# Performance work log

Measured on AMD Instinct MI355X. Metric: run time of the kernel, lower is better.

## Reference

```python
import jax, jax.numpy as jnp
import numpy as np

N = 320   # batch of events
D = 64    # features per event
P = 1000  # permutation_count (hard-coded in module)


def setup_inputs() -> dict:
    key = jax.random.key(0)
    k1, k2, k3 = jax.random.split(key, 3)
    data = jax.random.normal(k1, (N, D), dtype=jnp.float32)
    particle_types = jax.random.randint(k2, (N,), 0, 2, dtype=jnp.int32)
    # quantum permutations: 1000 independent random permutations of [0, N)
    perms = jax.vmap(lambda k: jax.random.permutation(k, N))(jax.random.split(k3, P)).astype(jnp.int32)
    return {
        "data": data,
        "fermion_antisymmetry": jnp.float32(-1.0),
        "boson_symmetry": jnp.float32(1.0),
        "particle_types": particle_types,
        "perms": perms,
    }


def reference(data, fermion_antisymmetry, boson_symmetry, particle_types, perms):
    n = data.shape[0]
    tf = particle_types  # [n]
    # statistics factor matrix F[i,j]: fermion-fermion -> -1 param, boson-boson -> +1 param, mixed -> 1.0
    ff = (tf[:, None] == 0) & (tf[None, :] == 0)
    bb = (tf[:, None] == 1) & (tf[None, :] == 1)
    F = jnp.where(ff, fermion_antisymmetry, jnp.where(bb, boson_symmetry, jnp.float32(1.0)))  # [n,n]

    ar = jnp.arange(n)
    gathered = data[perms]                      # [P,n,d] = data[perm[i]]
    fac = F[ar[None, :], perms]                 # [P,n]   = F[i, perm[i]]
    same = perms == ar[None, :]                 # i == perm[i]: keep original row unscaled
    perm_data = jnp.where(same[..., None], gathered, fac[..., None] * gathered)  # [P,n,d]

    all_data = jnp.concatenate([data[None], perm_data], axis=0)  # [P+1,n,d]; row 0 = original

    # pairwise Euclidean norms via Gram trick (avoids [P+1,n,n,d] diff tensor)
    sn = jnp.sum(all_data * all_data, axis=-1)                   # [P+1,n]
    gram = jnp.einsum('pnd,pmd->pnm', all_data, all_data)        # [P+1,n,n]
    sq = jnp.maximum(sn[:, :, None] + sn[:, None, :] - 2.0 * gram, 0.0)

    iu, ju = jnp.triu_indices(n, k=1)
    vals = F[iu, ju][None, :] * jnp.sqrt(sq[:, iu, ju])          # [P+1, n*(n-1)/2]
    # torch.var default is unbiased (ddof=1)
    stats = jnp.var(vals, axis=1, ddof=1)                        # [P+1]
    return stats  # stats[0] = original test statistic, stats[1:] = permutation null distribution
```

## Files before the change

kernel.cpp:

```cpp
#include <hip/hip_runtime.h>
#include <math.h>

#define NN 320
#define DD 64
#define ROWF (NN * 2)
#define NPERM 1001
#define KPB 4
#define NBLK ((NPERM + KPB - 1) / KPB)
#define NW 10
#define NITER 20
#define NPAIRF ((double)(NN * (NN - 1) / 2))


__global__ __launch_bounds__(NN) void dah_kernel(const float* __restrict__ data,
                                                 float2* __restrict__ DAH,
                                                 double* __restrict__ srow,
                                                 double* __restrict__ rsda) {
    __shared__ float rowa[DD];
    __shared__ double cr[5];
    const int a = blockIdx.x;
    const int t = threadIdx.x;
    if (t < DD) rowa[t] = data[a * DD + t];
    __syncthreads();
    const float* rb = data + t * DD;
    float g = 0.f, sa = 0.f, st = 0.f;
#pragma unroll
    for (int k = 0; k < DD; k += 4) {
        const float4 x = *(const float4*)(rb + k);
        const float r0 = rowa[k], r1 = rowa[k + 1], r2 = rowa[k + 2], r3 = rowa[k + 3];
        g  = fmaf(r0, x.x, g);   g  = fmaf(r1, x.y, g);
        g  = fmaf(r2, x.z, g);   g  = fmaf(r3, x.w, g);
        sa = fmaf(r0, r0, sa);   sa = fmaf(r1, r1, sa);
        sa = fmaf(r2, r2, sa);   sa = fmaf(r3, r3, sa);
        st = fmaf(x.x, x.x, st); st = fmaf(x.y, x.y, st);
        st = fmaf(x.z, x.z, st); st = fmaf(x.w, x.w, st);
    }
    const float sum = sa + st;
    const float dp = sqrtf(fmaxf(fmaf(-2.f, g, sum), 0.f));
    const float dm = sqrtf(fmaxf(fmaf( 2.f, g, sum), 0.f));
    const float da = 0.5f * (dp + dm);
    const float dh = 0.5f * (dp - dm);
    DAH[(size_t)a * NN + t] = make_float2(da, dh);

    double cd = (double)da;
    for (int off = 32; off; off >>= 1) cd += __shfl_down(cd, off, 64);
    const int wid = t >> 6, lane = t & 63;
    if (lane == 0) cr[wid] = cd;
    __syncthreads();
    if (t == 0) {
        double tot = 0.0;
#pragma unroll
        for (int i = 0; i < 5; ++i) tot += cr[i];
        rsda[a] = tot;
        srow[a] = (double)sa;
    }
}

__global__ __launch_bounds__(1024) void qf_kernel(const float* __restrict__ data,
                                                  const int* __restrict__ types,
                                                  const int* __restrict__ perms,
                                                  const float* __restrict__ fermp,
                                                  const float* __restrict__ bosp,
                                                  const float* __restrict__ DAHf,
                                                  const double* __restrict__ srow,
                                                  const double* __restrict__ rsda,
                                                  float* __restrict__ out) {
    __shared__ unsigned cb[KPB][2 * NW];
    __shared__ __align__(16) float rcoef[NN * 20];
    __shared__ float ysh[KPB][4][DD];
    __shared__ double red[16][12];
    __shared__ double redS[16], redC[16], scal[KPB];

    const int pg = blockIdx.x;
    const int t  = threadIdx.x;
    const int strip  = t & 63;
    const int rowoff = t >> 6;

    const float* gp = DAHf + (size_t)rowoff * ROWF + 2 * strip;
    float2 m0 = *(const float2*)(gp);
    float2 m1 = *(const float2*)(gp + 128);
    float2 m2 = *(const float2*)(gp + 256);
    float2 m3 = *(const float2*)(gp + 384);
    float2 m4 = *(const float2*)(gp + 512);

    if (t < KPB * 2 * NW) ((unsigned*)cb)[t] = 0u;
    __syncthreads();
    const float Fv = *fermp, Bv = *bosp;
    if (t < NN) {
        const int i  = t;
        const int ti = types[i];
#pragma unroll
        for (int k = 0; k < KPB; ++k) {
            int p = pg * KPB + k; if (p >= NPERM) p = NPERM - 1;
            const int a  = (p == 0) ? i : perms[(size_t)(p - 1) * NN + i];
            const int ta = types[a];
            float u = 1.f;
            if (a != i) u = (ti == 0 && ta == 0) ? Fv : ((ti == 1 && ta == 1) ? Bv : 1.f);
            if (u < 0.f) atomicOr(&cb[k][a >> 5], 1u << (a & 31));
            if (ti == 0) atomicOr(&cb[k][NW + (a >> 5)], 1u << (a & 31));
        }
    }
    __syncthreads();

    for (int j = t; j < NN * KPB; j += 1024) {
        const int r = j >> 2, k = j & 3;
        const unsigned ubit = (cb[k][r >> 5]        >> (r & 31)) & 1u;
        const unsigned qbit = (cb[k][NW + (r >> 5)] >> (r & 31)) & 1u;
        const float u = ubit ? -1.f : 1.f;
        *(float4*)&rcoef[(r * 5 + k) * 4] =
            make_float4(u, qbit ? 1.f : 0.f, qbit ? u : 0.f, 0.f);
    }

    float ub[KPB][5], qb[KPB][5], vb[KPB][5];
#pragma unroll
    for (int k = 0; k < KPB; ++k) {
#pragma unroll
        for (int e = 0; e < 5; ++e) {
            const int w = (strip >> 5) + 2 * e, b = strip & 31;
            const float u = ((cb[k][w] >> b) & 1u) ? -1.f : 1.f;
            const bool  q = ((cb[k][NW + w] >> b) & 1u) != 0u;
            ub[k][e] = u;
            qb[k][e] = q ? 1.f : 0.f;
            vb[k][e] = q ? u : 0.f;
        }
    }
    __syncthreads();

    float A2[KPB] = {0.f, 0.f, 0.f, 0.f};
    float A3[KPB] = {0.f, 0.f, 0.f, 0.f};
    float A4[KPB] = {0.f, 0.f, 0.f, 0.f};

    auto row_compute = [&](const float* ap) {
#pragma unroll
        for (int k = 0; k < KPB; ++k) {
            const float4 rp = *(const float4*)(ap + 4 * k);
            float r2 = ub[k][0] * m0.y;
            float r3 = qb[k][0] * m0.x;
            float r4 = vb[k][0] * m0.y;
            r2 = fmaf(ub[k][1], m1.y, r2); r3 = fmaf(qb[k][1], m1.x, r3); r4 = fmaf(vb[k][1], m1.y, r4);
            r2 = fmaf(ub[k][2], m2.y, r2); r3 = fmaf(qb[k][2], m2.x, r3); r4 = fmaf(vb[k][2], m2.y, r4);
            r2 = fmaf(ub[k][3], m3.y, r2); r3 = fmaf(qb[k][3], m3.x, r3); r4 = fmaf(vb[k][3], m3.y, r4);
            r2 = fmaf(ub[k][4], m4.y, r2); r3 = fmaf(qb[k][4], m4.x, r3); r4 = fmaf(vb[k][4], m4.y, r4);
            A2[k] = fmaf(rp.x, r2, A2[k]);
            A3[k] = fmaf(rp.y, r3, A3[k]);
            A4[k] = fmaf(rp.z, r4, A4[k]);
        }
    };

    for (int it = 0; it < NITER; ++it) {
        const float* gq = (it < NITER - 1) ? (gp + 16 * ROWF) : gp;
        const float2 n0 = *(const float2*)(gq);
        const float2 n1 = *(const float2*)(gq + 128);
        const float2 n2 = *(const float2*)(gq + 256);
        const float2 n3 = *(const float2*)(gq + 384);
        const float2 n4 = *(const float2*)(gq + 512);
        row_compute(rcoef + (it * 16 + rowoff) * 20);
        m0 = n0; m1 = n1; m2 = n2; m3 = n3; m4 = n4;
        gp = gq;
    }

    {
        const int k = t >> 8, sub = t & 255;
        const int j = sub >> 6, d = sub & 63;
        float acc = 0.f;
        for (int r = j * 80; r < j * 80 + 80; ++r)
            acc = fmaf(rcoef[(r * 5 + k) * 4], data[(size_t)r * DD + d], acc);
        ysh[k][j][d] = acc;
    }

    double rd[12];
#pragma unroll
    for (int k = 0; k < KPB; ++k) {
        rd[k]     = (double)A2[k];
        rd[4 + k] = (double)A3[k];
        rd[8 + k] = (double)A4[k];
    }
    for (int off = 32; off; off >>= 1) {
#pragma unroll
        for (int j = 0; j < 12; ++j) rd[j] += __shfl_down(rd[j], off, 64);
    }
    const int wid = t >> 6, lane = t & 63;
    if (lane == 0) {
#pragma unroll
        for (int j = 0; j < 12; ++j) red[wid][j] = rd[j];
    }

    {
        double sS = 0.0, sC = 0.0;
        if (t < NN) { sS = srow[t]; sC = rsda[t]; }
        for (int off = 32; off; off >>= 1) {
            sS += __shfl_down(sS, off, 64);
            sC += __shfl_down(sC, off, 64);
        }
        if (lane == 0) { redS[wid] = sS; redC[wid] = sC; }
    }
    __syncthreads();

    if (t < KPB * 64) {
        const int k = t >> 6, d = t & 63;
        const float yv = (ysh[k][0][d] + ysh[k][1][d]) + (ysh[k][2][d] + ysh[k][3][d]);
        double yy = (double)yv * (double)yv;
        for (int off = 32; off; off >>= 1) yy += __shfl_down(yy, off, 64);
        if ((t & 63) == 0) scal[k] = yy;
    }
    __syncthreads();

    if (t == 0) {
        double S = 0.0, C0 = 0.0;
#pragma unroll
        for (int w = 0; w < 16; ++w) { S += redS[w]; C0 += redC[w]; }
#pragma unroll
        for (int k = 0; k < KPB; ++k) {
            const int p = pg * KPB + k;
            if (p < NPERM) {
                double T2 = 0.0, T3 = 0.0, T4 = 0.0;
#pragma unroll
                for (int w = 0; w < 16; ++w) {
                    T2 += red[w][k];
                    T3 += red[w][4 + k];
                    T4 += red[w][8 + k];
                }
                const double SV  = 0.5 * (C0 + T2 - 2.0 * T3 - 2.0 * T4);
                const double SV2 = (double)NN * S - scal[k];
                out[p] = (float)((SV2 - SV * SV / NPAIRF) / (NPAIRF - 1.0));
            }
        }
    }
}

extern "C" void kernel_launch(void* const* d_in, const int* in_sizes, int n_in,
                              void* d_out, int out_size, void* d_ws, size_t ws_size,
                              hipStream_t stream) {
    const float* data  = (const float*)d_in[0];
    const float* fermp = (const float*)d_in[1];
    const float* bosp  = (const float*)d_in[2];
    const int*   types = (const int*)d_in[3];
    const int*   perms = (const int*)d_in[4];
    float* out = (float*)d_out;

    double* srow = (double*)d_ws;
    double* rsda = (double*)((char*)d_ws + 4096);
    float2* DAH  = (float2*)((char*)d_ws + 1048576);

    dah_kernel<<<NN, NN, 0, stream>>>(data, DAH, srow, rsda);
    qf_kernel<<<NBLK, 1024, 0, stream>>>(data, types, perms, fermp, bosp,
                                         (const float*)DAH, srow, rsda, out);
}
```

Baseline: 98.41 us.

## Split permutation kernel over row chunks and add final reduction kernel

The main kernel's row loop is split across four blocks per permutation group (a 2D grid), each handling a quarter of the rows. Each block writes partial sums and partial y-vectors to workspace. A new final kernel combines the partials and computes the variance statistic. The aim is more blocks and less serial work per block, to improve GPU occupancy. The cost is redundant per-block setup (bitmask building), an extra kernel launch and extra global traffic for the partials.

After: 132.5 us. 1.35x slower.

```diff
diff --git a/kernel.cpp b/kernel.cpp
--- a/kernel.cpp
+++ b/kernel.cpp
@@ -6,9 +6,11 @@
 #define ROWF (NN * 2)
 #define NPERM 1001
 #define KPB 4
-#define NBLK ((NPERM + KPB - 1) / KPB)
+#define NPG ((NPERM + KPB - 1) / KPB)
+#define RSPLIT 4
+#define RCH (NN / RSPLIT)
+#define NSLOT (RCH / 16)
 #define NW 10
-#define NITER 20
 #define NPAIRF ((double)(NN * (NN - 1) / 2))
 
 
@@ -62,21 +64,21 @@
                                                   const float* __restrict__ fermp,
                                                   const float* __restrict__ bosp,
                                                   const float* __restrict__ DAHf,
-                                                  const double* __restrict__ srow,
-                                                  const double* __restrict__ rsda,
-                                                  float* __restrict__ out) {
+                                                  double* __restrict__ part,
+                                                  float* __restrict__ ypart) {
     __shared__ unsigned cb[KPB][2 * NW];
-    __shared__ __align__(16) float rcoef[NN * 20];
+    __shared__ __align__(16) float rcoef[RCH * 20];
     __shared__ float ysh[KPB][4][DD];
     __shared__ double red[16][12];
-    __shared__ double redS[16], redC[16], scal[KPB];
-
-    const int pg = blockIdx.x;
-    const int t  = threadIdx.x;
+
+    const int pg   = blockIdx.x;
+    const int rc   = blockIdx.y;
+    const int row0 = rc * RCH;
+    const int t    = threadIdx.x;
     const int strip  = t & 63;
     const int rowoff = t >> 6;
 
-    const float* gp = DAHf + (size_t)rowoff * ROWF + 2 * strip;
+    const float* gp = DAHf + (size_t)(row0 + rowoff) * ROWF + 2 * strip;
     float2 m0 = *(const float2*)(gp);
     float2 m1 = *(const float2*)(gp + 128);
     float2 m2 = *(const float2*)(gp + 256);
@@ -102,12 +104,13 @@
     }
     __syncthreads();
 
-    for (int j = t; j < NN * KPB; j += 1024) {
+    for (int j = t; j < RCH * KPB; j += 1024) {
         const int r = j >> 2, k = j & 3;
-        const unsigned ubit = (cb[k][r >> 5]        >> (r & 31)) & 1u;
-        const unsigned qbit = (cb[k][NW + (r >> 5)] >> (r & 31)) & 1u;
+        const int a = row0 + r;
+        const unsigned ubit = (cb[k][a >> 5]        >> (a & 31)) & 1u;
+        const unsigned qbit = (cb[k][NW + (a >> 5)] >> (a & 31)) & 1u;
         const float u = ubit ? -1.f : 1.f;
-        *(float4*)&rcoef[(r * 5 + k) * 4] =
+        *(float4*)&rcoef[r * 20 + k * 4] =
             make_float4(u, qbit ? 1.f : 0.f, qbit ? u : 0.f, 0.f);
     }
 
@@ -147,14 +150,14 @@
         }
     };
 
-    for (int it = 0; it < NITER; ++it) {
-        const float* gq = (it < NITER - 1) ? (gp + 16 * ROWF) : gp;
+    for (int slot = 0; slot < NSLOT; ++slot) {
+        const float* gq = (slot < NSLOT - 1) ? (gp + 16 * ROWF) : gp;
         const float2 n0 = *(const float2*)(gq);
         const float2 n1 = *(const float2*)(gq + 128);
         const float2 n2 = *(const float2*)(gq + 256);
         const float2 n3 = *(const float2*)(gq + 384);
         const float2 n4 = *(const float2*)(gq + 512);
-        row_compute(rcoef + (it * 16 + rowoff) * 20);
+        row_compute(rcoef + (slot * 16 + rowoff) * 20);
         m0 = n0; m1 = n1; m2 = n2; m3 = n3; m4 = n4;
         gp = gq;
     }
@@ -163,9 +166,15 @@
         const int k = t >> 8, sub = t & 255;
         const int j = sub >> 6, d = sub & 63;
         float acc = 0.f;
-        for (int r = j * 80; r < j * 80 + 80; ++r)
-            acc = fmaf(rcoef[(r * 5 + k) * 4], data[(size_t)r * DD + d], acc);
+        for (int r = j * 20; r < j * 20 + 20; ++r)
+            acc = fmaf(rcoef[r * 20 + k * 4], data[(size_t)(row0 + r) * DD + d], acc);
         ysh[k][j][d] = acc;
+    }
+    __syncthreads();
+    if (t < KPB * DD) {
+        const int k = t / DD, d = t % DD;
+        const float yp = (ysh[k][0][d] + ysh[k][1][d]) + (ysh[k][2][d] + ysh[k][3][d]);
+        ypart[(((size_t)pg * RSPLIT + rc) * KPB + k) * DD + d] = yp;
     }
 
     double rd[12];
@@ -184,46 +193,62 @@
 #pragma unroll
         for (int j = 0; j < 12; ++j) red[wid][j] = rd[j];
     }
-
-    {
+    __syncthreads();
+    if (t == 0) {
+        double* dst = part + ((size_t)pg * RSPLIT + rc) * 16;
+#pragma unroll
+        for (int j = 0; j < 12; ++j) {
+            double v = 0.0;
+            for (int w = 0; w < 16; ++w) v += red[w][j];
+            dst[j] = v;
+        }
+    }
+}
+
+__global__ __launch_bounds__(256) void final_kernel(const double* __restrict__ srow,
+                                                    const double* __restrict__ rsda,
+                                                    const double* __restrict__ part,
+                                                    const float* __restrict__ ypart,
+                                                    float* __restrict__ out) {
+    __shared__ double sSh, sCh;
+    const int pg = blockIdx.x;
+    const int t  = threadIdx.x;
+    const int wid = t >> 6, lane = t & 63;
+
+    if (wid == 0) {
         double sS = 0.0, sC = 0.0;
-        if (t < NN) { sS = srow[t]; sC = rsda[t]; }
+#pragma unroll
+        for (int i = 0; i < 5; ++i) { sS += srow[lane + 64 * i]; sC += rsda[lane + 64 * i]; }
         for (int off = 32; off; off >>= 1) {
             sS += __shfl_down(sS, off, 64);
             sC += __shfl_down(sC, off, 64);
         }
-        if (lane == 0) { redS[wid] = sS; redC[wid] = sC; }
-    }
-    __syncthreads();
-
-    if (t < KPB * 64) {
-        const int k = t >> 6, d = t & 63;
-        const float yv = (ysh[k][0][d] + ysh[k][1][d]) + (ysh[k][2][d] + ysh[k][3][d]);
-        double yy = (double)yv * (double)yv;
-        for (int off = 32; off; off >>= 1) yy += __shfl_down(yy, off, 64);
-        if ((t & 63) == 0) scal[k] = yy;
-    }
-    __syncthreads();
-
-    if (t == 0) {
-        double S = 0.0, C0 = 0.0;
-#pragma unroll
-        for (int w = 0; w < 16; ++w) { S += redS[w]; C0 += redC[w]; }
-#pragma unroll
-        for (int k = 0; k < KPB; ++k) {
-            const int p = pg * KPB + k;
-            if (p < NPERM) {
-                double T2 = 0.0, T3 = 0.0, T4 = 0.0;
-#pragma unroll
-                for (int w = 0; w < 16; ++w) {
-                    T2 += red[w][k];
-                    T3 += red[w][4 + k];
-                    T4 += red[w][8 + k];
-                }
-                const double SV  = 0.5 * (C0 + T2 - 2.0 * T3 - 2.0 * T4);
-                const double SV2 = (double)NN * S - scal[k];
-                out[p] = (float)((SV2 - SV * SV / NPAIRF) / (NPAIRF - 1.0));
+        if (lane == 0) { sSh = sS; sCh = sC; }
+    }
+    __syncthreads();
+
+    float yv = 0.f;
+#pragma unroll
+    for (int rc = 0; rc < RSPLIT; ++rc)
+        yv += ypart[(((size_t)pg * RSPLIT + rc) * KPB + wid) * DD + lane];
+    double yy = (double)yv * (double)yv;
+    for (int off = 32; off; off >>= 1) yy += __shfl_down(yy, off, 64);
+
+    if (lane == 0) {
+        const int p = pg * KPB + wid;
+        if (p < NPERM) {
+            const double S = sSh, C0 = sCh;
+            double T2 = 0.0, T3 = 0.0, T4 = 0.0;
+#pragma unroll
+            for (int rc = 0; rc < RSPLIT; ++rc) {
+                const double* pb = part + ((size_t)pg * RSPLIT + rc) * 16;
+                T2 += pb[wid];
+                T3 += pb[4 + wid];
+                T4 += pb[8 + wid];
             }
+            const double SV  = 0.5 * (C0 + T2 - 2.0 * T3 - 2.0 * T4);
+            const double SV2 = (double)NN * S - yy;
+            out[p] = (float)((SV2 - SV * SV / NPAIRF) / (NPAIRF - 1.0));
         }
     }
 }
@@ -238,11 +263,14 @@
     const int*   perms = (const int*)d_in[4];
     float* out = (float*)d_out;
 
-    double* srow = (double*)d_ws;
-    double* rsda = (double*)((char*)d_ws + 4096);
-    float2* DAH  = (float2*)((char*)d_ws + 1048576);
+    double* srow  = (double*)d_ws;
+    double* rsda  = (double*)((char*)d_ws + 4096);
+    double* part  = (double*)((char*)d_ws + 8192);
+    float*  ypart = (float*)((char*)d_ws + 270336);
+    float2* DAH   = (float2*)((char*)d_ws + 2097152);
 
     dah_kernel<<<NN, NN, 0, stream>>>(data, DAH, srow, rsda);
-    qf_kernel<<<NBLK, 1024, 0, stream>>>(data, types, perms, fermp, bosp,
-                                         (const float*)DAH, srow, rsda, out);
-}
+    qf_kernel<<<dim3(NPG, RSPLIT), 1024, 0, stream>>>(data, types, perms, fermp, bosp,
+                                                      (const float*)DAH, part, ypart);
+    final_kernel<<<NPG, 256, 0, stream>>>(srow, rsda, part, ypart, out);
+}
```
